# Kernel tuning notes

Measured on AMD Instinct MI355X. Metric: run time of the kernel, lower is better.

The kernel has to match this reference:

```python
import jax, jax.numpy as jnp
import numpy as np

B, S, D, H, E, K = 1, 2048, 1024, 16, 8, 2
DK = D // H          # 64 per-head key dim
FF = 4 * D           # 4096 expert hidden
EPS = 1e-5


def rmsnorm(x, scale):
    rms = jnp.sqrt(jnp.mean(x * x, axis=-1, keepdims=True) + EPS)
    return scale * (x / rms)


def setup_inputs() -> dict:
    key = jax.random.key(0)
    ks = jax.random.split(key, 12)
    std = 0.02
    x = jax.random.normal(ks[0], (B, S, D), dtype=jnp.float32)
    # causal mask: masked_fill where mask == 0
    self_attn_mask = jnp.tril(jnp.ones((S, S), dtype=jnp.int32))
    scale_attn = jnp.ones((D,), dtype=jnp.float32)
    scale_ffn = jnp.ones((D,), dtype=jnp.float32)
    # per-head projections, stacked: [H, DK, D] (torch Linear weight layout [out,in])
    Wq = jax.random.normal(ks[1], (H, DK, D), dtype=jnp.float32) * std
    Wk = jax.random.normal(ks[2], (H, DK, D), dtype=jnp.float32) * std
    Wv = jax.random.normal(ks[3], (H, DK, D), dtype=jnp.float32) * std
    Wo = jax.random.normal(ks[4], (D, D), dtype=jnp.float32) * std
    Wg = jax.random.normal(ks[5], (E, D), dtype=jnp.float32) * std   # router gate
    W_in = jax.random.normal(ks[6], (E, FF, D), dtype=jnp.float32) * std   # expert linear
    W_v = jax.random.normal(ks[7], (E, FF, D), dtype=jnp.float32) * std    # expert linear_v
    W_out = jax.random.normal(ks[8], (E, D, FF), dtype=jnp.float32) * std  # expert linear_out
    return {
        'x': x, 'self_attn_mask': self_attn_mask,
        'scale_attn': scale_attn, 'Wq': Wq, 'Wk': Wk, 'Wv': Wv, 'Wo': Wo,
        'scale_ffn': scale_ffn, 'Wg': Wg, 'W_in': W_in, 'W_v': W_v, 'W_out': W_out,
    }


def reference(x, self_attn_mask, scale_attn, Wq, Wk, Wv, Wo, scale_ffn, Wg, W_in, W_v, W_out):
    # --- self attention (pre-RMSNorm) ---
    normed = rmsnorm(x, scale_attn)
    q = jnp.einsum('bsd,hkd->bhsk', normed, Wq)
    k = jnp.einsum('bsd,hkd->bhsk', normed, Wk)
    v = jnp.einsum('bsd,hkd->bhsk', normed, Wv)
    attn = jnp.einsum('bhsk,bhtk->bhst', q, k) / np.sqrt(DK).astype(np.float32)
    attn = jnp.where(self_attn_mask[None, None] == 0, -jnp.inf, attn)
    attn = jax.nn.softmax(attn, axis=-1)
    ctx = jnp.einsum('bhst,bhtk->bhsk', attn, v)
    ctx = ctx.transpose(0, 2, 1, 3).reshape(x.shape[0], x.shape[1], D)  # concat heads
    a1 = ctx @ Wo.T
    x = x + a1
    # --- MoE (pre-RMSNorm) ---
    normed = rmsnorm(x, scale_ffn)
    router_logits = normed @ Wg.T                       # [B,S,E]
    router_probs = jax.nn.softmax(router_logits, axis=-1)
    gate, idx = jax.lax.top_k(router_probs, K)          # [B,S,K]
    gate = gate / jnp.sum(gate, axis=-1, keepdims=True)
    # combine weights per expert: sum of renormalized gates over selected slots
    onehot = (idx[..., None] == jnp.arange(E)).astype(x.dtype)  # [B,S,K,E]
    combine = jnp.sum(gate[..., None] * onehot, axis=2)         # [B,S,E]
    # all-expert dense FFN (faithful to the masked dense loop in torch)
    g = jax.nn.gelu(jnp.einsum('bsd,efd->bsef', normed, W_in), approximate=False)
    val = jnp.einsum('bsd,efd->bsef', normed, W_v)
    eo = jnp.einsum('bsef,edf->bsed', g * val, W_out)           # [B,S,E,D]
    moe_out = jnp.einsum('bse,bsed->bsd', combine, eo)
    out = x + moe_out
    return (out, router_probs)
```

## Files before the change

### kernel.cpp

```cpp
#include <hip/hip_runtime.h>
#include <hip/hip_bf16.h>
#include <math.h>

typedef unsigned int u32;
typedef unsigned short u16;
using bf16x8 = __attribute__((ext_vector_type(8))) short;
using f32x4 = __attribute__((ext_vector_type(4))) float;

#define MFMA_BF16(a, b, c) __builtin_amdgcn_mfma_f32_16x16x32_bf16((a), (b), (c), 0, 0, 0)
#define VMCNT8() asm volatile("s_waitcnt vmcnt(8)" ::: "memory")
#define VMCNT6() asm volatile("s_waitcnt vmcnt(6)" ::: "memory")
#define VMCNT0() asm volatile("s_waitcnt vmcnt(0)" ::: "memory")
#define SBAR() __builtin_amdgcn_s_barrier()
#define SCHED0() __builtin_amdgcn_sched_barrier(0)

constexpr int kS = 2048, kD = 1024, kH = 16, kE = 8, kFF = 4096;
constexpr int kSlotCap = 5120;
constexpr int kMaxTiles = 40;
constexpr int kChunk = 8;

__device__ __forceinline__ u16 bf16_rne(float f) {
  u32 u = __float_as_uint(f);
  u32 r = (u + 0x7fffu + ((u >> 16) & 1u)) >> 16;
  return (u16)r;
}
__device__ __forceinline__ float bf16_f32(u16 h) { return __uint_as_float(((u32)h) << 16); }
__device__ __forceinline__ u32 pack_hl(float x) {
  u16 hi = bf16_rne(x);
  u16 lo = bf16_rne(x - bf16_f32(hi));
  return ((u32)lo << 16) | (u32)hi;
}
__device__ __forceinline__ void unpack8(const u32* t, bf16x8& h, bf16x8& l) {
#pragma unroll
  for (int j = 0; j < 8; j++) {
    h[j] = (short)(t[j] & 0xffffu);
    l[j] = (short)(t[j] >> 16);
  }
}
__device__ __forceinline__ void gload_lds16(const void* g, void* l) {
  __builtin_amdgcn_global_load_lds((const __attribute__((address_space(1))) u32*)g,
                                   (__attribute__((address_space(3))) u32*)l, 16, 0, 0);
}

__global__ __launch_bounds__(256) void pack_dp3(const float* __restrict__ Wq,
                                                const float* __restrict__ Wk,
                                                const float* __restrict__ Wv,
                                                u16* __restrict__ o) {
  int i = blockIdx.x * 256 + threadIdx.x;
  if (i >= 3072 * 1024) return;
  int n = i >> 10, k = i & 1023;
  float v = (n < 1024) ? Wq[i] : (n < 2048) ? Wk[i - 1024 * 1024] : Wv[i - 2048 * 1024];
  u16 hi = bf16_rne(v);
  u16 lo = bf16_rne(v - bf16_f32(hi));
  size_t b = (size_t)n * 2048 + (size_t)(k >> 5) * 64 + (k & 31);
  o[b] = hi;
  o[b + 32] = lo;
}
__global__ __launch_bounds__(256) void pack_dp1(const float* __restrict__ W,
                                                u16* __restrict__ o, int n_elem) {
  int i = blockIdx.x * 256 + threadIdx.x;
  if (i >= n_elem) return;
  int k = i & 1023, n = i >> 10;
  float v = W[i];
  u16 hi = bf16_rne(v);
  u16 lo = bf16_rne(v - bf16_f32(hi));
  size_t b = (size_t)n * 2048 + (size_t)(k >> 5) * 64 + (k & 31);
  o[b] = hi;
  o[b + 32] = lo;
}
__global__ __launch_bounds__(256) void pack_winv(const float* __restrict__ Wi,
                                                 const float* __restrict__ Wv,
                                                 u16* __restrict__ o) {
  size_t i8 = (size_t)blockIdx.x * 256 + threadIdx.x;
  if (i8 >= (size_t)kE * 8192 * 1024 / 8) return;
  size_t flat = i8 * 8;
  int e = (int)(flat >> 23);
  int r = (int)(flat & ((1u << 23) - 1));
  int n = r >> 10, k = r & 1023;
  const float* src = (n < 4096) ? Wi + ((size_t)e * 4096 + n) * 1024 + k
                                : Wv + ((size_t)e * 4096 + (n - 4096)) * 1024 + k;
  float4 a = *(const float4*)src;
  float4 b = *(const float4*)(src + 4);
  u16 rr[8] = {bf16_rne(a.x), bf16_rne(a.y), bf16_rne(a.z), bf16_rne(a.w),
               bf16_rne(b.x), bf16_rne(b.y), bf16_rne(b.z), bf16_rne(b.w)};
  *(uint4*)(o + flat) = *(uint4*)rr;
}
__global__ __launch_bounds__(256) void pack_bf16_kernel(const float* __restrict__ w,
                                                        u16* __restrict__ o, int n8) {
  int i = blockIdx.x * 256 + threadIdx.x;
  if (i >= n8) return;
  const float4* s = (const float4*)w + (size_t)i * 2;
  float4 a = s[0], b = s[1];
  u16 r[8] = {bf16_rne(a.x), bf16_rne(a.y), bf16_rne(a.z), bf16_rne(a.w),
              bf16_rne(b.x), bf16_rne(b.y), bf16_rne(b.z), bf16_rne(b.w)};
  *(uint4*)(o + (size_t)i * 8) = *(uint4*)r;
}

template <int MODE>
__global__ __launch_bounds__(256) void rmsnorm_kernel(
    const float* __restrict__ x, const float* __restrict__ scale,
    u16* __restrict__ odp, float* __restrict__ of32, u16* __restrict__ ob16) {
  const int s = blockIdx.x;
  const float* row = x + (size_t)s * kD;
  const int c = threadIdx.x * 4;
  float4 v = *(const float4*)(row + c);
  float ss = v.x * v.x + v.y * v.y + v.z * v.z + v.w * v.w;
#pragma unroll
  for (int m = 32; m; m >>= 1) ss += __shfl_xor(ss, m);
  __shared__ float wsum[4];
  if ((threadIdx.x & 63) == 0) wsum[threadIdx.x >> 6] = ss;
  __syncthreads();
  float tot = wsum[0] + wsum[1] + wsum[2] + wsum[3];
  float rinv = 1.0f / sqrtf(tot * (1.0f / kD) + 1e-5f);
  float4 sc = *(const float4*)(scale + c);
  float n[4] = {v.x * rinv * sc.x, v.y * rinv * sc.y, v.z * rinv * sc.z, v.w * rinv * sc.w};
  if (MODE == 0) {
    u16 hv[4], lv[4];
#pragma unroll
    for (int j = 0; j < 4; j++) {
      hv[j] = bf16_rne(n[j]);
      lv[j] = bf16_rne(n[j] - bf16_f32(hv[j]));
    }
    u16* o = odp + (size_t)s * 2048 + (size_t)(c >> 5) * 64 + (c & 31);
    *(uint2*)o = *(uint2*)hv;
    *(uint2*)(o + 32) = *(uint2*)lv;
  } else {
    *(float4*)(of32 + (size_t)s * kD + c) = make_float4(n[0], n[1], n[2], n[3]);
    u16* o = ob16 + (size_t)s * kD + c;
    o[0] = bf16_rne(n[0]); o[1] = bf16_rne(n[1]); o[2] = bf16_rne(n[2]); o[3] = bf16_rne(n[3]);
  }
}

template <int APK, int OUT>
__global__ __launch_bounds__(256) void gemm_dp(
    const void* __restrict__ Av, const u16* __restrict__ Bdp,
    const float* __restrict__ resid, int K,
    u32* __restrict__ oq, u32* __restrict__ ok, u32* __restrict__ ov,
    float* __restrict__ of) {
  __shared__ u16 As[2][128 * 64];
  __shared__ u16 Bs[2][128 * 64];
  const int tid = threadIdx.x, w = tid >> 6, l = tid & 63;
  const int m0 = blockIdx.y * 128, n0 = blockIdx.x * 128;
  const int wr = (w >> 1) * 64, wc = (w & 1) * 64;
  const char* Ab = (const char*)Av;
  const char* Bb = (const char*)Bdp;
  const size_t rowb = (size_t)K * 4;

  size_t asrc[4], bsrc[4];
  int dst[4];
#pragma unroll
  for (int i = 0; i < 4; i++) {
    int fl = i * 256 + tid;
    int row = fl >> 3, cb = fl & 7;
    size_t coff = (size_t)((cb ^ (row & 7)) * 16);
    asrc[i] = (size_t)(m0 + row) * rowb + coff;
    bsrc[i] = (size_t)(n0 + row) * rowb + coff;
    dst[i] = fl * 16;
  }

  f32x4 zero = {0.f, 0.f, 0.f, 0.f};
  f32x4 acc[4][4];
#pragma unroll
  for (int i = 0; i < 4; i++)
#pragma unroll
    for (int j = 0; j < 4; j++) acc[i][j] = zero;

  auto stage = [&](int buf, int s) {
    const char* ap = Ab + (size_t)s * 128;
    const char* bp = Bb + (size_t)s * 128;
#pragma unroll
    for (int i = 0; i < 4; i++) {
      gload_lds16(ap + asrc[i], (char*)&As[buf][0] + dst[i]);
      gload_lds16(bp + bsrc[i], (char*)&Bs[buf][0] + dst[i]);
    }
  };

  const int NS = K / 32;
  stage(0, 0);
  for (int s = 0; s < NS; s++) {
    const int cur = s & 1;
    const bool lastit = (s == NS - 1);
    if (!lastit) stage(cur ^ 1, s + 1);
    if (!lastit) VMCNT8(); else VMCNT0();
    SBAR();
    SCHED0();
    bf16x8 ah[4], al[4], bh[4], bl[4];
    const int g = l >> 4;
    if (APK) {
      const u32* At = (const u32*)&As[cur][0];
#pragma unroll
      for (int mi = 0; mi < 4; mi++) {
        int row = wr + mi * 16 + (l & 15);
        u32 t[8];
        *(uint4*)t = *(const uint4*)&At[row * 32 + (((2 * g) ^ (row & 7)) * 4)];
        *(uint4*)(t + 4) = *(const uint4*)&At[row * 32 + (((2 * g + 1) ^ (row & 7)) * 4)];
        unpack8(t, ah[mi], al[mi]);
      }
    } else {
#pragma unroll
      for (int mi = 0; mi < 4; mi++) {
        int row = wr + mi * 16 + (l & 15);
        ah[mi] = *(const bf16x8*)&As[cur][row * 64 + ((g ^ (row & 7)) * 8)];
        al[mi] = *(const bf16x8*)&As[cur][row * 64 + (((4 + g) ^ (row & 7)) * 8)];
      }
    }
#pragma unroll
    for (int ni = 0; ni < 4; ni++) {
      int row = wc + ni * 16 + (l & 15);
      bh[ni] = *(const bf16x8*)&Bs[cur][row * 64 + ((g ^ (row & 7)) * 8)];
      bl[ni] = *(const bf16x8*)&Bs[cur][row * 64 + (((4 + g) ^ (row & 7)) * 8)];
    }
#pragma unroll
    for (int mi = 0; mi < 4; mi++)
#pragma unroll
      for (int ni = 0; ni < 4; ni++) {
        f32x4 c = acc[mi][ni];
        c = MFMA_BF16(al[mi], bl[ni], c);
        c = MFMA_BF16(al[mi], bh[ni], c);
        c = MFMA_BF16(ah[mi], bl[ni], c);
        c = MFMA_BF16(ah[mi], bh[ni], c);
        acc[mi][ni] = c;
      }
    SCHED0();
    if (!lastit) SBAR();
  }

  if (OUT == 0) {
    u32* dstp;
    int nb;
    if (n0 < 1024) { dstp = oq; nb = n0; }
    else if (n0 < 2048) { dstp = ok; nb = n0 - 1024; }
    else { dstp = ov; nb = n0 - 2048; }
#pragma unroll
    for (int mi = 0; mi < 4; mi++)
#pragma unroll
      for (int ni = 0; ni < 4; ni++)
#pragma unroll
        for (int r = 0; r < 4; r++) {
          int row = m0 + wr + mi * 16 + ((l >> 4) << 2) + r;
          int col = nb + wc + ni * 16 + (l & 15);
          dstp[(size_t)row * 1024 + col] = pack_hl(acc[mi][ni][r]);
        }
  } else {
#pragma unroll
    for (int mi = 0; mi < 4; mi++)
#pragma unroll
      for (int ni = 0; ni < 4; ni++)
#pragma unroll
        for (int r = 0; r < 4; r++) {
          int row = m0 + wr + mi * 16 + ((l >> 4) << 2) + r;
          int col = n0 + wc + ni * 16 + (l & 15);
          of[(size_t)row * 1024 + col] = resid[(size_t)row * 1024 + col] + acc[mi][ni][r];
        }
  }
}

__global__ __launch_bounds__(256) void attn_kernel(
    const u32* __restrict__ Qp, const u32* __restrict__ Kp, const u32* __restrict__ Vp,
    float* __restrict__ Opart, float* __restrict__ mpart, float* __restrict__ lpart) {
  constexpr int LDK = 68;
  __shared__ u32 Ks[64 * LDK];
  __shared__ u32 Vs[64 * LDK];
  __shared__ u32 Ps[64 * LDK];
  const int tid = threadIdx.x, w = tid >> 6, l = tid & 63;
  int b = blockIdx.x, qt, c;
  if (b < 8) { qt = b; c = 0; }
  else if (b < 24) { qt = 8 + ((b - 8) >> 1); c = (b - 8) & 1; }
  else if (b < 48) { qt = 16 + (b - 24) / 3; c = (b - 24) % 3; }
  else { qt = 24 + ((b - 48) >> 2); c = (b - 48) & 3; }
  const int hh = blockIdx.y;
  const int q0 = qt * 64, hc = hh * 64;
  const int kt0 = c * kChunk;
  const int kt1 = min(kt0 + kChunk, qt + 1);

  bf16x8 qh[2], ql[2];
  {
    const int qrow = q0 + w * 16 + (l & 15);
#pragma unroll
    for (int kk = 0; kk < 2; kk++) {
      u32 t[8];
      const u32* p = Qp + (size_t)qrow * kD + hc + kk * 32 + ((l >> 4) << 3);
      *(uint4*)t = *(const uint4*)p;
      *(uint4*)(t + 4) = *(const uint4*)(p + 4);
      unpack8(t, qh[kk], ql[kk]);
    }
  }
  float mrun[4], lrun[4];
  f32x4 zero = {0.f, 0.f, 0.f, 0.f};
  f32x4 oacc[4];
#pragma unroll
  for (int r = 0; r < 4; r++) { mrun[r] = -3.0e38f; lrun[r] = 0.f; }
#pragma unroll
  for (int vb = 0; vb < 4; vb++) oacc[vb] = zero;

  const int trow = tid >> 2, c0v = (tid & 3) * 16;
  const u32* gKb = Kp + hc + c0v;
  const u32* gVb = Vp + hc + c0v;
  uint4 kr[4], vr[4];
  {
    const u32* gK = gKb + (size_t)(kt0 * 64 + trow) * kD;
    kr[0] = *(const uint4*)gK; kr[1] = *(const uint4*)(gK + 4);
    kr[2] = *(const uint4*)(gK + 8); kr[3] = *(const uint4*)(gK + 12);
    const u32* gV = gVb + (size_t)(kt0 * 64 + trow) * kD;
    vr[0] = *(const uint4*)gV; vr[1] = *(const uint4*)(gV + 4);
    vr[2] = *(const uint4*)(gV + 8); vr[3] = *(const uint4*)(gV + 12);
  }

  for (int kt = kt0; kt < kt1; kt++) {
    {
      u32* sK = Ks + trow * LDK + c0v;
      *(uint4*)sK = kr[0]; *(uint4*)(sK + 4) = kr[1];
      *(uint4*)(sK + 8) = kr[2]; *(uint4*)(sK + 12) = kr[3];
#pragma unroll
      for (int j = 0; j < 4; j++) {
        Vs[(c0v + j * 4 + 0) * LDK + trow] = vr[j].x;
        Vs[(c0v + j * 4 + 1) * LDK + trow] = vr[j].y;
        Vs[(c0v + j * 4 + 2) * LDK + trow] = vr[j].z;
        Vs[(c0v + j * 4 + 3) * LDK + trow] = vr[j].w;
      }
    }
    __syncthreads();
    if (kt + 1 < kt1) {
      const u32* gK = gKb + (size_t)((kt + 1) * 64 + trow) * kD;
      kr[0] = *(const uint4*)gK; kr[1] = *(const uint4*)(gK + 4);
      kr[2] = *(const uint4*)(gK + 8); kr[3] = *(const uint4*)(gK + 12);
      const u32* gV = gVb + (size_t)((kt + 1) * 64 + trow) * kD;
      vr[0] = *(const uint4*)gV; vr[1] = *(const uint4*)(gV + 4);
      vr[2] = *(const uint4*)(gV + 8); vr[3] = *(const uint4*)(gV + 12);
    }

    f32x4 sfr[4];
#pragma unroll
    for (int kb = 0; kb < 4; kb++) {
      f32x4 sa = zero;
#pragma unroll
      for (int kk = 0; kk < 2; kk++) {
        u32 t[8];
        bf16x8 kh, kl;
        const u32* p = Ks + (kb * 16 + (l & 15)) * LDK + kk * 32 + ((l >> 4) << 3);
        *(uint4*)t = *(const uint4*)p;
        *(uint4*)(t + 4) = *(const uint4*)(p + 4);
        unpack8(t, kh, kl);
        sa = MFMA_BF16(ql[kk], kl, sa);
        sa = MFMA_BF16(ql[kk], kh, sa);
        sa = MFMA_BF16(qh[kk], kl, sa);
        sa = MFMA_BF16(qh[kk], kh, sa);
      }
      sfr[kb] = sa * 0.125f;
    }
    if (kt == qt) {
#pragma unroll
      for (int kb = 0; kb < 4; kb++) {
        int t = kt * 64 + kb * 16 + (l & 15);
#pragma unroll
        for (int r = 0; r < 4; r++) {
          int qq = q0 + w * 16 + ((l >> 4) << 2) + r;
          if (t > qq) sfr[kb][r] = -3.0e38f;
        }
      }
    }
#pragma unroll
    for (int r = 0; r < 4; r++) {
      float mx = fmaxf(fmaxf(sfr[0][r], sfr[1][r]), fmaxf(sfr[2][r], sfr[3][r]));
#pragma unroll
      for (int mm = 1; mm < 16; mm <<= 1) mx = fmaxf(mx, __shfl_xor(mx, mm));
      float mnew = fmaxf(mrun[r], mx);
      float sf = __expf(mrun[r] - mnew);
      mrun[r] = mnew;
      float rs = 0.f;
#pragma unroll
      for (int kb = 0; kb < 4; kb++) {
        float p = __expf(sfr[kb][r] - mnew);
        sfr[kb][r] = p;
        rs += p;
      }
#pragma unroll
      for (int mm = 1; mm < 16; mm <<= 1) rs += __shfl_xor(rs, mm);
      lrun[r] = lrun[r] * sf + rs;
#pragma unroll
      for (int vb = 0; vb < 4; vb++) oacc[vb][r] *= sf;
    }
#pragma unroll
    for (int kb = 0; kb < 4; kb++)
#pragma unroll
      for (int r = 0; r < 4; r++)
        Ps[(w * 16 + ((l >> 4) << 2) + r) * LDK + kb * 16 + (l & 15)] = pack_hl(sfr[kb][r]);
#pragma unroll
    for (int ks = 0; ks < 2; ks++) {
      bf16x8 ph, pl;
      {
        u32 t[8];
        const u32* pp = Ps + (w * 16 + (l & 15)) * LDK + ks * 32 + ((l >> 4) << 3);
        *(uint4*)t = *(const uint4*)pp;
        *(uint4*)(t + 4) = *(const uint4*)(pp + 4);
        unpack8(t, ph, pl);
      }
#pragma unroll
      for (int vb = 0; vb < 4; vb++) {
        u32 t2[8];
        bf16x8 vh, vl;
        const u32* pv = Vs + (vb * 16 + (l & 15)) * LDK + ks * 32 + ((l >> 4) << 3);
        *(uint4*)t2 = *(const uint4*)pv;
        *(uint4*)(t2 + 4) = *(const uint4*)(pv + 4);
        unpack8(t2, vh, vl);
        f32x4 cc = oacc[vb];
        cc = MFMA_BF16(pl, vl, cc);
        cc = MFMA_BF16(pl, vh, cc);
        cc = MFMA_BF16(ph, vl, cc);
        cc = MFMA_BF16(ph, vh, cc);
        oacc[vb] = cc;
      }
    }
    __syncthreads();
  }

  const int p = (qt * 16 + hh) * 4 + c;
  float* Po = Opart + (size_t)p * 4096;
#pragma unroll
  for (int vb = 0; vb < 4; vb++)
#pragma unroll
    for (int r = 0; r < 4; r++) {
      int rl = w * 16 + ((l >> 4) << 2) + r;
      int cl = vb * 16 + (l & 15);
      Po[rl * 64 + cl] = oacc[vb][r];
    }
  if ((l & 15) == 0) {
#pragma unroll
    for (int r = 0; r < 4; r++) {
      int rl = w * 16 + ((l >> 4) << 2) + r;
      mpart[p * 64 + rl] = mrun[r];
      lpart[p * 64 + rl] = lrun[r];
    }
  }
}

__global__ __launch_bounds__(256) void attn_merge(
    const float* __restrict__ Opart, const float* __restrict__ mpart,
    const float* __restrict__ lpart, u32* __restrict__ Op) {
  const int qt = blockIdx.x, hh = blockIdx.y;
  const int nch = (qt + kChunk) >> 3;
  const int t = threadIdx.x;
  const int row = t >> 2;
  const int c0 = (t & 3) * 16;
  const int pbase = (qt * 16 + hh) * 4;
  float M = -3.0e38f;
  for (int c = 0; c < nch; c++) M = fmaxf(M, mpart[(pbase + c) * 64 + row]);
  float den = 0.f;
  float acc[16];
#pragma unroll
  for (int j = 0; j < 16; j++) acc[j] = 0.f;
  for (int c = 0; c < nch; c++) {
    float wgt = __expf(mpart[(pbase + c) * 64 + row] - M);
    den += wgt * lpart[(pbase + c) * 64 + row];
    const float* po = Opart + (size_t)(pbase + c) * 4096 + row * 64 + c0;
#pragma unroll
    for (int j = 0; j < 16; j += 4) {
      float4 v = *(const float4*)(po + j);
      acc[j] += wgt * v.x; acc[j + 1] += wgt * v.y;
      acc[j + 2] += wgt * v.z; acc[j + 3] += wgt * v.w;
    }
  }
  float inv = 1.f / den;
  u32* dst = Op + (size_t)(qt * 64 + row) * kD + hh * 64 + c0;
#pragma unroll
  for (int j = 0; j < 16; j++) dst[j] = pack_hl(acc[j] * inv);
}

__global__ __launch_bounds__(256) void router_kernel(
    const float* __restrict__ normed, const float* __restrict__ Wg,
    float* __restrict__ probs, float* __restrict__ gates,
    int* __restrict__ experts, int* __restrict__ counts) {
  const int w = threadIdx.x >> 6, l = threadIdx.x & 63;
  const int s = blockIdx.x * 4 + w;
  float lg[kE];
  const float* row = normed + (size_t)s * kD;
#pragma unroll
  for (int e = 0; e < kE; e++) {
    const float* wg = Wg + (size_t)e * kD;
    float a = 0.f;
    for (int d = l; d < kD; d += 64) a += row[d] * wg[d];
#pragma unroll
    for (int m = 32; m; m >>= 1) a += __shfl_xor(a, m);
    lg[e] = a;
  }
  if (l == 0) {
    float mx = lg[0];
#pragma unroll
    for (int e = 1; e < kE; e++) mx = fmaxf(mx, lg[e]);
    float p[kE], sum = 0.f;
#pragma unroll
    for (int e = 0; e < kE; e++) { p[e] = __expf(lg[e] - mx); sum += p[e]; }
    float inv = 1.f / sum;
#pragma unroll
    for (int e = 0; e < kE; e++) { p[e] *= inv; probs[(size_t)s * kE + e] = p[e]; }
    int i1 = 0;
#pragma unroll
    for (int e = 1; e < kE; e++) if (lg[e] > lg[i1]) i1 = e;
    int i2 = (i1 == 0) ? 1 : 0;
#pragma unroll
    for (int e = 0; e < kE; e++) if (e != i1 && lg[e] > lg[i2]) i2 = e;
    float den = 1.f / (p[i1] + p[i2]);
    gates[s * 2] = p[i1] * den;
    gates[s * 2 + 1] = p[i2] * den;
    experts[s * 2] = i1;
    experts[s * 2 + 1] = i2;
    atomicAdd(&counts[i1], 1);
    atomicAdd(&counts[i2], 1);
  }
}

__global__ void moe_init(int* counts) {
  if (threadIdx.x < kE) counts[threadIdx.x] = 0;
}
__global__ void moe_scan(const int* __restrict__ counts, int* __restrict__ ebase,
                         int* __restrict__ cursor, int2* __restrict__ tmap) {
  if (threadIdx.x == 0) {
    int acc = 0, t = 0;
    for (int e = 0; e < kE; e++) {
      ebase[e] = acc;
      cursor[e] = acc;
      int nt = (counts[e] + 127) >> 7;
      for (int i = 0; i < nt; i++) tmap[t++] = make_int2(e, i * 128);
      acc += nt << 7;
    }
    ebase[kE] = acc;
    for (; t < kMaxTiles; t++) tmap[t] = make_int2(-1, 0);
  }
}
__global__ void moe_fill(const int* __restrict__ experts, int* __restrict__ cursor,
                         int* __restrict__ slot_list, int* __restrict__ slot_of) {
  int s = blockIdx.x * 256 + threadIdx.x;
  if (s >= kS) return;
  for (int k = 0; k < 2; k++) {
    int e = experts[s * 2 + k];
    int pos = atomicAdd(&cursor[e], 1);
    slot_list[pos] = s;
    slot_of[s * 2 + k] = pos;
  }
}

__global__ __launch_bounds__(256) void moe_mmA(
    const u16* __restrict__ A, const u16* __restrict__ Bg,
    const int* __restrict__ slot_list, const int* __restrict__ counts,
    const int* __restrict__ ebase, const int2* __restrict__ tmap,
    u16* __restrict__ Uraw) {
  int2 tm = tmap[blockIdx.y];
  const int e = tm.x;
  if (e < 0) return;
  const int base = ebase[e], Me = counts[e], m0 = tm.y;
  const int n0 = blockIdx.x * 128;
  __shared__ u16 As[2][128 * 64];
  __shared__ u16 Bs[2][128 * 64];
  const int tid = threadIdx.x, w = tid >> 6, l = tid & 63;
  const int wr = (w >> 1) * 64, wc = (w & 1) * 64;
  const char* Ab = (const char*)A;
  const char* Bb = (const char*)(Bg + ((size_t)e * 8192) * 1024);

  size_t asrc[4], bsrc[4];
  int dst[4];
#pragma unroll
  for (int i = 0; i < 4; i++) {
    int fl = i * 256 + tid;
    int row = fl >> 3, cb = fl & 7;
    size_t coff = (size_t)((cb ^ (row & 7)) * 16);
    int mr = m0 + row;
    if (mr > Me - 1) mr = Me - 1;
    int ar = slot_list[base + mr];
    asrc[i] = (size_t)ar * 2048 + coff;
    bsrc[i] = (size_t)(n0 + row) * 2048 + coff;
    dst[i] = fl * 16;
  }

  f32x4 zero = {0.f, 0.f, 0.f, 0.f};
  f32x4 acc[4][4];
#pragma unroll
  for (int i = 0; i < 4; i++)
#pragma unroll
    for (int j = 0; j < 4; j++) acc[i][j] = zero;

  auto stage = [&](int buf, int s) {
    const size_t so = (size_t)s * 128;
#pragma unroll
    for (int i = 0; i < 4; i++) {
      gload_lds16(Ab + so + asrc[i], (char*)&As[buf][0] + dst[i]);
      gload_lds16(Bb + so + bsrc[i], (char*)&Bs[buf][0] + dst[i]);
    }
  };

  const int NS = kD / 64;
  stage(0, 0);
  for (int s = 0; s < NS; s++) {
    const int cur = s & 1;
    const bool lastit = (s == NS - 1);
    if (!lastit) stage(cur ^ 1, s + 1);
    if (!lastit) VMCNT8(); else VMCNT0();
    SBAR();
    SCHED0();
#pragma unroll
    for (int kk = 0; kk < 2; kk++) {
      const int g = kk * 4 + (l >> 4);
      bf16x8 af[4], bfr[4];
#pragma unroll
      for (int mi = 0; mi < 4; mi++) {
        int row = wr + mi * 16 + (l & 15);
        af[mi] = *(const bf16x8*)&As[cur][row * 64 + ((g ^ (row & 7)) * 8)];
      }
#pragma unroll
      for (int ni = 0; ni < 4; ni++) {
        int row = wc + ni * 16 + (l & 15);
        bfr[ni] = *(const bf16x8*)&Bs[cur][row * 64 + ((g ^ (row & 7)) * 8)];
      }
#pragma unroll
      for (int mi = 0; mi < 4; mi++)
#pragma unroll
        for (int ni = 0; ni < 4; ni++) acc[mi][ni] = MFMA_BF16(af[mi], bfr[ni], acc[mi][ni]);
    }
    SCHED0();
    if (!lastit) SBAR();
  }

#pragma unroll
  for (int mi = 0; mi < 4; mi++)
#pragma unroll
    for (int r = 0; r < 4; r++) {
      int ml = m0 + wr + mi * 16 + ((l >> 4) << 2) + r;
      if (ml >= Me) continue;
      size_t rb = (size_t)(base + ml) * 8192;
#pragma unroll
      for (int ni = 0; ni < 4; ni++) {
        int col = n0 + wc + ni * 16 + (l & 15);
        Uraw[rb + col] = bf16_rne(acc[mi][ni][r]);
      }
    }
}

__global__ __launch_bounds__(256) void gelu_mul(const u16* __restrict__ Uraw,
                                                u16* __restrict__ H) {
  size_t i8 = (size_t)blockIdx.x * 256 + threadIdx.x;
  if (i8 >= (size_t)kSlotCap * kFF / 8) return;
  int row = (int)(i8 >> 9);
  int j8 = ((int)i8 & 511) * 8;
  const u16* up = Uraw + (size_t)row * 8192 + j8;
  uint4 uu = *(const uint4*)up;
  uint4 vv = *(const uint4*)(up + 4096);
  const u16* ue = (const u16*)&uu;
  const u16* ve = (const u16*)&vv;
  u16 o[8];
#pragma unroll
  for (int k = 0; k < 8; k++) {
    float u = bf16_f32(ue[k]), v = bf16_f32(ve[k]);
    float ge = 0.5f * u * (1.0f + erff(u * 0.70710678118654752f));
    o[k] = bf16_rne(ge * v);
  }
  *(uint4*)(H + (size_t)row * kFF + j8) = *(uint4*)o;
}

__global__ __launch_bounds__(256) void moe_mm2(
    const u16* __restrict__ H, const u16* __restrict__ Bg,
    const int* __restrict__ counts, const int* __restrict__ ebase,
    const int2* __restrict__ tmap, float* __restrict__ eo) {
  int2 tm = tmap[blockIdx.y];
  const int e = tm.x;
  if (e < 0) return;
  const int base = ebase[e], Me = counts[e], m0 = tm.y;
  const int n0 = blockIdx.x * 64;
  __shared__ u16 As[2][128 * 64];
  __shared__ u16 Bs[2][64 * 64];
  const int tid = threadIdx.x, w = tid >> 6, l = tid & 63;
  const int wr = (w >> 1) * 64, wc = (w & 1) * 32;
  const char* Ab = (const char*)H;
  const char* Bb = (const char*)(Bg + (size_t)e * kD * kFF);

  size_t asrc[4], bsrc[2];
  int adst[4], bdst[2];
#pragma unroll
  for (int i = 0; i < 4; i++) {
    int fl = i * 256 + tid;
    int row = fl >> 3, cb = fl & 7;
    int mr = m0 + row;
    if (mr > Me - 1) mr = Me - 1;
    asrc[i] = (size_t)(base + mr) * 8192 + (size_t)((cb ^ (row & 7)) * 16);
    adst[i] = fl * 16;
  }
#pragma unroll
  for (int i = 0; i < 2; i++) {
    int fl = i * 256 + tid;
    int row = fl >> 3, cb = fl & 7;
    bsrc[i] = (size_t)(n0 + row) * 8192 + (size_t)((cb ^ (row & 7)) * 16);
    bdst[i] = fl * 16;
  }

  f32x4 zero = {0.f, 0.f, 0.f, 0.f};
  f32x4 acc[4][2];
#pragma unroll
  for (int i = 0; i < 4; i++)
#pragma unroll
    for (int j = 0; j < 2; j++) acc[i][j] = zero;

  auto stage = [&](int buf, int s) {
    const size_t so = (size_t)s * 128;
#pragma unroll
    for (int i = 0; i < 4; i++) gload_lds16(Ab + so + asrc[i], (char*)&As[buf][0] + adst[i]);
#pragma unroll
    for (int i = 0; i < 2; i++) gload_lds16(Bb + so + bsrc[i], (char*)&Bs[buf][0] + bdst[i]);
  };

  const int NS = kFF / 64;
  stage(0, 0);
  for (int s = 0; s < NS; s++) {
    const int cur = s & 1;
    const bool lastit = (s == NS - 1);
    if (!lastit) stage(cur ^ 1, s + 1);
    if (!lastit) VMCNT6(); else VMCNT0();
    SBAR();
    SCHED0();
#pragma unroll
    for (int kk = 0; kk < 2; kk++) {
      const int g = kk * 4 + (l >> 4);
      bf16x8 af[4], bfr[2];
#pragma unroll
      for (int mi = 0; mi < 4; mi++) {
        int row = wr + mi * 16 + (l & 15);
        af[mi] = *(const bf16x8*)&As[cur][row * 64 + ((g ^ (row & 7)) * 8)];
      }
#pragma unroll
      for (int ni = 0; ni < 2; ni++) {
        int row = wc + ni * 16 + (l & 15);
        bfr[ni] = *(const bf16x8*)&Bs[cur][row * 64 + ((g ^ (row & 7)) * 8)];
      }
#pragma unroll
      for (int mi = 0; mi < 4; mi++)
#pragma unroll
        for (int ni = 0; ni < 2; ni++) acc[mi][ni] = MFMA_BF16(af[mi], bfr[ni], acc[mi][ni]);
    }
    SCHED0();
    if (!lastit) SBAR();
  }

#pragma unroll
  for (int mi = 0; mi < 4; mi++)
#pragma unroll
    for (int r = 0; r < 4; r++) {
      int ml = m0 + wr + mi * 16 + ((l >> 4) << 2) + r;
      if (ml >= Me) continue;
      size_t rb = (size_t)(base + ml) * kD;
#pragma unroll
      for (int ni = 0; ni < 2; ni++) {
        int col = n0 + wc + ni * 16 + (l & 15);
        eo[rb + col] = acc[mi][ni][r];
      }
    }
}

__global__ __launch_bounds__(256) void combine_kernel(
    const float* __restrict__ h, const float* __restrict__ eo,
    const float* __restrict__ gates, const int* __restrict__ slot_of,
    float* __restrict__ out) {
  const int s = blockIdx.x;
  const float g0 = gates[s * 2], g1 = gates[s * 2 + 1];
  const int p0 = slot_of[s * 2], p1 = slot_of[s * 2 + 1];
  const int c = threadIdx.x * 4;
  float4 hv = *(const float4*)(h + (size_t)s * kD + c);
  float4 e0 = *(const float4*)(eo + (size_t)p0 * kD + c);
  float4 e1 = *(const float4*)(eo + (size_t)p1 * kD + c);
  float4 o;
  o.x = hv.x + g0 * e0.x + g1 * e1.x;
  o.y = hv.y + g0 * e0.y + g1 * e1.y;
  o.z = hv.z + g0 * e0.z + g1 * e1.z;
  o.w = hv.w + g0 * e0.w + g1 * e1.w;
  *(float4*)(out + (size_t)s * kD + c) = o;
}

extern "C" void kernel_launch(void* const* d_in, const int* in_sizes, int n_in,
                              void* d_out, int out_size, void* d_ws, size_t ws_size,
                              hipStream_t stream) {
  (void)in_sizes; (void)n_in; (void)out_size; (void)ws_size;
  const float* x = (const float*)d_in[0];
  const float* scale_attn = (const float*)d_in[2];
  const float* Wq = (const float*)d_in[3];
  const float* Wk = (const float*)d_in[4];
  const float* Wv = (const float*)d_in[5];
  const float* Wo = (const float*)d_in[6];
  const float* scale_ffn = (const float*)d_in[7];
  const float* Wg = (const float*)d_in[8];
  const float* W_in = (const float*)d_in[9];
  const float* W_vv = (const float*)d_in[10];
  const float* W_out = (const float*)d_in[11];
  float* out = (float*)d_out;
  float* probs = out + (size_t)kS * kD;

  char* wsb = (char*)d_ws;
  size_t off = 0;
  auto alloc = [&](size_t bytes) -> void* {
    void* p = wsb + off;
    off += (bytes + 255) & ~(size_t)255;
    return p;
  };
  const size_t SDu = (size_t)kS * kD;
  u16* Uraw = (u16*)wsb;
  u16* normA_dp = (u16*)alloc(SDu * 4);
  u32* qpk = (u32*)alloc(SDu * 4);
  u32* kpk = (u32*)alloc(SDu * 4);
  u32* vpk = (u32*)alloc(SDu * 4);
  u32* ctxpk = (u32*)alloc(SDu * 4);
  u16* Wqkv_dp = (u16*)alloc((size_t)3072 * 2048 * 2);
  u16* Wo_dp = (u16*)alloc((size_t)1024 * 2048 * 2);
  float* normFf = (float*)alloc(SDu * 4);
  float* eo = (float*)alloc((size_t)kSlotCap * kD * 4);
  float* h = (float*)alloc(SDu * 4);
  u16* normFb = (u16*)alloc(SDu * 2);
  u16* Winv_bf = (u16*)alloc((size_t)kE * 8192 * 1024 * 2);
  u16* Wout_bf = (u16*)alloc((size_t)kE * kD * kFF * 2);
  u16* H = (u16*)alloc((size_t)kSlotCap * kFF * 2);
  float* Opart = (float*)alloc((size_t)2048 * 4096 * 4);
  float* mpart = (float*)alloc((size_t)2048 * 64 * 4);
  float* lpart = (float*)alloc((size_t)2048 * 64 * 4);
  float* gates = (float*)alloc(kS * 2 * 4);
  int* experts = (int*)alloc(kS * 2 * 4);
  int* slot_of = (int*)alloc(kS * 2 * 4);
  int* slot_list = (int*)alloc(kSlotCap * 4);
  int* counts = (int*)alloc(64);
  int* ebase = (int*)alloc(64);
  int* cursor = (int*)alloc(64);
  int2* tmap = (int2*)alloc(kMaxTiles * 8);

  pack_dp3<<<(3072 * 1024) / 256, 256, 0, stream>>>(Wq, Wk, Wv, Wqkv_dp);
  pack_dp1<<<(1024 * 1024) / 256, 256, 0, stream>>>(Wo, Wo_dp, 1024 * 1024);
  pack_winv<<<(int)((size_t)kE * 8192 * 1024 / 8 / 256), 256, 0, stream>>>(W_in, W_vv, Winv_bf);
  const int n8o = (int)((size_t)kE * kD * kFF / 8);
  pack_bf16_kernel<<<(n8o + 255) / 256, 256, 0, stream>>>(W_out, Wout_bf, n8o);

  rmsnorm_kernel<0><<<kS, 256, 0, stream>>>(x, scale_attn, normA_dp, nullptr, nullptr);
  gemm_dp<0, 0><<<dim3(3072 / 128, kS / 128), 256, 0, stream>>>(
      normA_dp, Wqkv_dp, nullptr, kD, qpk, kpk, vpk, nullptr);
  attn_kernel<<<dim3(80, kH), 256, 0, stream>>>(qpk, kpk, vpk, Opart, mpart, lpart);
  attn_merge<<<dim3(kS / 64, kH), 256, 0, stream>>>(Opart, mpart, lpart, ctxpk);
  gemm_dp<1, 1><<<dim3(1024 / 128, kS / 128), 256, 0, stream>>>(
      ctxpk, Wo_dp, x, kD, nullptr, nullptr, nullptr, h);

  rmsnorm_kernel<1><<<kS, 256, 0, stream>>>(h, scale_ffn, nullptr, normFf, normFb);
  moe_init<<<1, 64, 0, stream>>>(counts);
  router_kernel<<<kS / 4, 256, 0, stream>>>(normFf, Wg, probs, gates, experts, counts);
  moe_scan<<<1, 64, 0, stream>>>(counts, ebase, cursor, tmap);
  moe_fill<<<kS / 256, 256, 0, stream>>>(experts, cursor, slot_list, slot_of);

  moe_mmA<<<dim3(8192 / 128, kMaxTiles), 256, 0, stream>>>(
      normFb, Winv_bf, slot_list, counts, ebase, tmap, Uraw);
  gelu_mul<<<(int)((size_t)kSlotCap * kFF / 8 / 256), 256, 0, stream>>>(Uraw, H);
  moe_mm2<<<dim3(kD / 64, kMaxTiles), 256, 0, stream>>>(
      H, Wout_bf, counts, ebase, tmap, eo);

  combine_kernel<<<kS, 256, 0, stream>>>(h, eo, gates, slot_of, out);
}
```

Before: 678.2 us.

## Interleave W_in/W_v rows and fuse GELU-multiply into expert up-projection epilogue

Interleaves W_in and W_v rows in the packed weight so adjacent output columns hold the gate and value for the same hidden unit. The up-projection epilogue then pairs them with a lane shuffle, applies erf-GELU and the multiply, and writes H directly. This removes the separate gelu_mul kernel and the bf16 Uraw round-trip. The K-step also shrinks from 64 to 32 with a new swizzle, halving LDS use but doubling barrier iterations, and the epilogue writes scattered 2-byte values from half the lanes.

Result: no change. 666.0 us (-1.8%).

```diff
diff --git a/kernel.cpp b/kernel.cpp
--- a/kernel.cpp
+++ b/kernel.cpp
@@ -10,6 +10,7 @@
 #define MFMA_BF16(a, b, c) __builtin_amdgcn_mfma_f32_16x16x32_bf16((a), (b), (c), 0, 0, 0)
 #define VMCNT8() asm volatile("s_waitcnt vmcnt(8)" ::: "memory")
 #define VMCNT6() asm volatile("s_waitcnt vmcnt(6)" ::: "memory")
+#define VMCNT4() asm volatile("s_waitcnt vmcnt(4)" ::: "memory")
 #define VMCNT0() asm volatile("s_waitcnt vmcnt(0)" ::: "memory")
 #define SBAR() __builtin_amdgcn_s_barrier()
 #define SCHED0() __builtin_amdgcn_sched_barrier(0)
@@ -77,8 +78,9 @@
   int e = (int)(flat >> 23);
   int r = (int)(flat & ((1u << 23) - 1));
   int n = r >> 10, k = r & 1023;
-  const float* src = (n < 4096) ? Wi + ((size_t)e * 4096 + n) * 1024 + k
-                                : Wv + ((size_t)e * 4096 + (n - 4096)) * 1024 + k;
+  const float* src = ((n & 1) == 0)
+                         ? Wi + ((size_t)e * 4096 + (n >> 1)) * 1024 + k
+                         : Wv + ((size_t)e * 4096 + (n >> 1)) * 1024 + k;
   float4 a = *(const float4*)src;
   float4 b = *(const float4*)(src + 4);
   u16 rr[8] = {bf16_rne(a.x), bf16_rne(a.y), bf16_rne(a.z), bf16_rne(a.w),
@@ -543,26 +545,27 @@
     const u16* __restrict__ A, const u16* __restrict__ Bg,
     const int* __restrict__ slot_list, const int* __restrict__ counts,
     const int* __restrict__ ebase, const int2* __restrict__ tmap,
-    u16* __restrict__ Uraw) {
+    u16* __restrict__ H) {
   int2 tm = tmap[blockIdx.y];
   const int e = tm.x;
   if (e < 0) return;
   const int base = ebase[e], Me = counts[e], m0 = tm.y;
   const int n0 = blockIdx.x * 128;
-  __shared__ u16 As[2][128 * 64];
-  __shared__ u16 Bs[2][128 * 64];
+  __shared__ u16 As[2][128 * 32];
+  __shared__ u16 Bs[2][128 * 32];
   const int tid = threadIdx.x, w = tid >> 6, l = tid & 63;
   const int wr = (w >> 1) * 64, wc = (w & 1) * 64;
   const char* Ab = (const char*)A;
   const char* Bb = (const char*)(Bg + ((size_t)e * 8192) * 1024);
 
-  size_t asrc[4], bsrc[4];
-  int dst[4];
-#pragma unroll
-  for (int i = 0; i < 4; i++) {
+  size_t asrc[2], bsrc[2];
+  int dst[2];
+#pragma unroll
+  for (int i = 0; i < 2; i++) {
     int fl = i * 256 + tid;
-    int row = fl >> 3, cb = fl & 7;
-    size_t coff = (size_t)((cb ^ (row & 7)) * 16);
+    int row = fl >> 2, cb = fl & 3;
+    int swz = cb ^ (row & 3) ^ ((row >> 2) & 3);
+    size_t coff = (size_t)swz * 16;
     int mr = m0 + row;
     if (mr > Me - 1) mr = Me - 1;
     int ar = slot_list[base + mr];
@@ -579,42 +582,41 @@
     for (int j = 0; j < 4; j++) acc[i][j] = zero;
 
   auto stage = [&](int buf, int s) {
-    const size_t so = (size_t)s * 128;
-#pragma unroll
-    for (int i = 0; i < 4; i++) {
+    const size_t so = (size_t)s * 64;
+#pragma unroll
+    for (int i = 0; i < 2; i++) {
       gload_lds16(Ab + so + asrc[i], (char*)&As[buf][0] + dst[i]);
       gload_lds16(Bb + so + bsrc[i], (char*)&Bs[buf][0] + dst[i]);
     }
   };
 
-  const int NS = kD / 64;
+  const int NS = kD / 32;
   stage(0, 0);
   for (int s = 0; s < NS; s++) {
     const int cur = s & 1;
     const bool lastit = (s == NS - 1);
     if (!lastit) stage(cur ^ 1, s + 1);
-    if (!lastit) VMCNT8(); else VMCNT0();
+    if (!lastit) VMCNT4(); else VMCNT0();
     SBAR();
     SCHED0();
-#pragma unroll
-    for (int kk = 0; kk < 2; kk++) {
-      const int g = kk * 4 + (l >> 4);
-      bf16x8 af[4], bfr[4];
-#pragma unroll
-      for (int mi = 0; mi < 4; mi++) {
-        int row = wr + mi * 16 + (l & 15);
-        af[mi] = *(const bf16x8*)&As[cur][row * 64 + ((g ^ (row & 7)) * 8)];
-      }
-#pragma unroll
-      for (int ni = 0; ni < 4; ni++) {
-        int row = wc + ni * 16 + (l & 15);
-        bfr[ni] = *(const bf16x8*)&Bs[cur][row * 64 + ((g ^ (row & 7)) * 8)];
-      }
-#pragma unroll
-      for (int mi = 0; mi < 4; mi++)
-#pragma unroll
-        for (int ni = 0; ni < 4; ni++) acc[mi][ni] = MFMA_BF16(af[mi], bfr[ni], acc[mi][ni]);
-    }
+    const int g = l >> 4;
+    bf16x8 af[4], bfr[4];
+#pragma unroll
+    for (int mi = 0; mi < 4; mi++) {
+      int row = wr + mi * 16 + (l & 15);
+      int m = (row & 3) ^ ((row >> 2) & 3);
+      af[mi] = *(const bf16x8*)&As[cur][row * 32 + ((g ^ m) * 8)];
+    }
+#pragma unroll
+    for (int ni = 0; ni < 4; ni++) {
+      int row = wc + ni * 16 + (l & 15);
+      int m = (row & 3) ^ ((row >> 2) & 3);
+      bfr[ni] = *(const bf16x8*)&Bs[cur][row * 32 + ((g ^ m) * 8)];
+    }
+#pragma unroll
+    for (int mi = 0; mi < 4; mi++)
+#pragma unroll
+      for (int ni = 0; ni < 4; ni++) acc[mi][ni] = MFMA_BF16(af[mi], bfr[ni], acc[mi][ni]);
     SCHED0();
     if (!lastit) SBAR();
   }
@@ -625,34 +627,18 @@
     for (int r = 0; r < 4; r++) {
       int ml = m0 + wr + mi * 16 + ((l >> 4) << 2) + r;
       if (ml >= Me) continue;
-      size_t rb = (size_t)(base + ml) * 8192;
+      size_t rb = (size_t)(base + ml) * 4096;
 #pragma unroll
       for (int ni = 0; ni < 4; ni++) {
         int col = n0 + wc + ni * 16 + (l & 15);
-        Uraw[rb + col] = bf16_rne(acc[mi][ni][r]);
-      }
-    }
-}
-
-__global__ __launch_bounds__(256) void gelu_mul(const u16* __restrict__ Uraw,
-                                                u16* __restrict__ H) {
-  size_t i8 = (size_t)blockIdx.x * 256 + threadIdx.x;
-  if (i8 >= (size_t)kSlotCap * kFF / 8) return;
-  int row = (int)(i8 >> 9);
-  int j8 = ((int)i8 & 511) * 8;
-  const u16* up = Uraw + (size_t)row * 8192 + j8;
-  uint4 uu = *(const uint4*)up;
-  uint4 vv = *(const uint4*)(up + 4096);
-  const u16* ue = (const u16*)&uu;
-  const u16* ve = (const u16*)&vv;
-  u16 o[8];
-#pragma unroll
-  for (int k = 0; k < 8; k++) {
-    float u = bf16_f32(ue[k]), v = bf16_f32(ve[k]);
-    float ge = 0.5f * u * (1.0f + erff(u * 0.70710678118654752f));
-    o[k] = bf16_rne(ge * v);
-  }
-  *(uint4*)(H + (size_t)row * kFF + j8) = *(uint4*)o;
+        float v0 = acc[mi][ni][r];
+        float pv = __shfl_xor(v0, 1);
+        if ((l & 1) == 0) {
+          float ge = 0.5f * v0 * (1.0f + erff(v0 * 0.70710678118654752f));
+          H[rb + (col >> 1)] = bf16_rne(ge * pv);
+        }
+      }
+    }
 }
 
 __global__ __launch_bounds__(256) void moe_mm2(
@@ -797,7 +783,6 @@
     return p;
   };
   const size_t SDu = (size_t)kS * kD;
-  u16* Uraw = (u16*)wsb;
   u16* normA_dp = (u16*)alloc(SDu * 4);
   u32* qpk = (u32*)alloc(SDu * 4);
   u32* kpk = (u32*)alloc(SDu * 4);
@@ -845,8 +830,7 @@
   moe_fill<<<kS / 256, 256, 0, stream>>>(experts, cursor, slot_list, slot_of);
 
   moe_mmA<<<dim3(8192 / 128, kMaxTiles), 256, 0, stream>>>(
-      normFb, Winv_bf, slot_list, counts, ebase, tmap, Uraw);
-  gelu_mul<<<(int)((size_t)kSlotCap * kFF / 8 / 256), 256, 0, stream>>>(Uraw, H);
+      normFb, Winv_bf, slot_list, counts, ebase, tmap, H);
   moe_mm2<<<dim3(kD / 64, kMaxTiles), 256, 0, stream>>>(
       H, Wout_bf, counts, ebase, tmap, eo);
 
```
